# Performance work log

Measured on AMD Instinct MI355X. Metric: run time of the kernel, lower is better.

Reference implementation:

```python
import jax, jax.numpy as jnp
import numpy as np

N = 100000   # nodes
E = 1600000  # edges (avg degree 16)
D = 32       # feature dim

def setup_inputs() -> dict:
    key = jax.random.key(0)
    k1, k2, k3, k4 = jax.random.split(key, 4)
    feat = jax.random.normal(k1, (N, D), dtype=jnp.float32)
    e_feat = jax.random.normal(k2, (E, 1), dtype=jnp.float32)
    src = jax.random.randint(k3, (E,), 0, N)
    dst = jax.random.randint(k4, (E,), 0, N)
    return {"feat": feat, "e_feat": e_feat, "src": src, "dst": dst}

def reference(feat, e_feat, src, dst):
    n = feat.shape[0]
    ones = jnp.ones(src.shape[0], dtype=feat.dtype)
    # degrees computed on the full graph (before self-loop removal), as in DGL code
    out_deg = jax.ops.segment_sum(ones, src, num_segments=n)
    in_deg = jax.ops.segment_sum(ones, dst, num_segments=n)
    src_norm = jnp.power(jnp.clip(out_deg, 1.0, None), -0.5)[:, None]  # [N,1]
    dst_norm = jnp.power(jnp.clip(in_deg, 1.0, None), -0.5)[:, None]   # [N,1]
    # remove_self_loop: mask out self-loop edges in the aggregation only
    mask = (src != dst).astype(feat.dtype)[:, None]                    # [E,1]
    # u_mul_e: gather normalized src features, multiply by edge weight
    msg = (feat * src_norm)[src] * (e_feat * mask)                     # [E,D]
    agg = jax.ops.segment_sum(msg, dst, num_segments=n)                # [N,D]
    out = feat - agg * dst_norm
    return jnp.sum(jnp.abs(out), axis=1)                               # [N]
```

## Files before the change

kernel.cpp:

```cpp
#include <hip/hip_runtime.h>

#define D 32
#define RANGE 128
#define RMAX 800
#define JC 512
#define CHUNKMAX 3200
#define CAP 2304
#define SJC 256
#define SCHUNKMAX 6400

__device__ __forceinline__ int scan512(int x, int* wp, int t) {
    int lane = t & 63, w = t >> 6;
    #pragma unroll
    for (int d = 1; d < 64; d <<= 1) {
        int y = __shfl_up(x, d, 64);
        if (lane >= d) x += y;
    }
    if (lane == 63) wp[w] = x;
    __syncthreads();
    int off = 0;
    #pragma unroll
    for (int i = 0; i < 7; i++) if (i < w) off += wp[i];
    return x + off;
}

__global__ __launch_bounds__(512) void fused_sort(
        const int* __restrict__ src, const int* __restrict__ dst,
        const float* __restrict__ ef,
        uint2* __restrict__ recs, unsigned* __restrict__ metaD,
        unsigned* __restrict__ srcs, unsigned* __restrict__ metaS,
        int E, int R, int chunk, int chunkS) {
    __shared__ __align__(16) char arena[32000];
    __shared__ int wp[8];
    int t = threadIdx.x;
    int* cnt = (int*)(arena + 25600);
    int* cur = (int*)(arena + 28800);

    if (blockIdx.x < JC) {
        int j = blockIdx.x;
        uint2* sd = (uint2*)arena;
        int e0 = j * chunk, e1 = min(E, e0 + chunk), cntE = e1 - e0;
        for (int i = t; i < RMAX; i += 512) cnt[i] = 0;
        __syncthreads();
        for (int e = e0 + 2 * t; e < e1; e += 1024) {
            if (e + 1 < e1) {
                int2 d2 = *(const int2*)(dst + e);
                atomicAdd(&cnt[d2.x >> 7], 1);
                atomicAdd(&cnt[d2.y >> 7], 1);
            } else {
                atomicAdd(&cnt[dst[e] >> 7], 1);
            }
        }
        __syncthreads();
        int v0 = cnt[t];
        int incl0 = scan512(v0, wp, t);
        int tot0 = wp[0] + wp[1] + wp[2] + wp[3] + wp[4] + wp[5] + wp[6] + wp[7];
        __syncthreads();
        int i1 = t + 512;
        int v1 = (i1 < RMAX) ? cnt[i1] : 0;
        int incl1 = scan512(v1, wp, t);
        cur[t] = incl0 - v0;
        if (i1 < RMAX) cur[i1] = tot0 + incl1 - v1;
        __syncthreads();
        for (int e = e0 + t; e < e1; e += 512) {
            int s = src[e], d = dst[e];
            float w = (s == d) ? 0.0f : ef[e];
            int pos = atomicAdd(&cur[d >> 7], 1);
            sd[pos] = make_uint2((unsigned)s | ((unsigned)(d & (RANGE - 1)) << 17),
                                 __float_as_uint(w));
        }
        __syncthreads();
        size_t baseE = (size_t)j * chunk;
        for (int i = t; i < cntE; i += 512) recs[baseE + i] = sd[i];
        for (int i = t; i < R; i += 512)
            metaD[(size_t)i * JC + j] =
                ((unsigned)(cur[i] - cnt[i]) << 16) | (unsigned)cnt[i];
    } else {
        int j = blockIdx.x - JC;
        unsigned* ids = (unsigned*)arena;
        int e0 = j * chunkS, e1 = min(E, e0 + chunkS), cntE = e1 - e0;
        for (int i = t; i < RMAX; i += 512) cnt[i] = 0;
        __syncthreads();
        for (int e = e0 + 2 * t; e < e1; e += 1024) {
            if (e + 1 < e1) {
                int2 s2 = *(const int2*)(src + e);
                atomicAdd(&cnt[s2.x >> 7], 1);
                atomicAdd(&cnt[s2.y >> 7], 1);
            } else {
                atomicAdd(&cnt[src[e] >> 7], 1);
            }
        }
        __syncthreads();
        int v0 = cnt[t];
        int incl0 = scan512(v0, wp, t);
        int tot0 = wp[0] + wp[1] + wp[2] + wp[3] + wp[4] + wp[5] + wp[6] + wp[7];
        __syncthreads();
        int i1 = t + 512;
        int v1 = (i1 < RMAX) ? cnt[i1] : 0;
        int incl1 = scan512(v1, wp, t);
        cur[t] = incl0 - v0;
        if (i1 < RMAX) cur[i1] = tot0 + incl1 - v1;
        __syncthreads();
        for (int e = e0 + t; e < e1; e += 512) {
            unsigned s = (unsigned)src[e];
            int pos = atomicAdd(&cur[s >> 7], 1);
            ids[pos] = s;
        }
        __syncthreads();
        size_t baseE = (size_t)j * chunkS;
        for (int i = t; i < cntE; i += 512) srcs[baseE + i] = ids[i];
        for (int i = t; i < R; i += 512)
            metaS[(size_t)j * R + i] =
                ((unsigned)(cur[i] - cnt[i]) << 16) | (unsigned)cnt[i];
    }
}

__device__ __forceinline__ unsigned short f2bf(float x) {
    unsigned u = __float_as_uint(x);
    u += 0x7FFFu + ((u >> 16) & 1u);
    return (unsigned short)(u >> 16);
}

__global__ __launch_bounds__(512) void srcnorm_convert(
        const unsigned* __restrict__ srcs, const unsigned* __restrict__ metaS,
        const float* __restrict__ feat, unsigned short* __restrict__ featb,
        int n, int R, int chunkS) {
    __shared__ int cnt[RANGE];
    __shared__ unsigned meta[SJC];
    int r = blockIdx.x, t = threadIdx.x;
    int base = r * RANGE, lim = min(n - base, RANGE);
    if (t < RANGE) cnt[t] = 0;
    if (t < SJC) meta[t] = metaS[(size_t)t * R + r];
    __syncthreads();
    int seg = t >> 1, sub = t & 1;
    {
        unsigned m = meta[seg];
        int st = m >> 16, c = m & 0xFFFFu;
        const unsigned* p = srcs + (size_t)seg * chunkS + st;
        for (int k = sub; k < c; k += 2)
            atomicAdd(&cnt[p[k] - (unsigned)base], 1);
    }
    __syncthreads();
    int total4 = lim * 8;
    for (int i = t; i < total4; i += 512) {
        int row = i >> 3;
        float sn = rsqrtf((float)max(cnt[row], 1));
        float4 f = ((const float4*)(feat + (size_t)(base + row) * D))[i & 7];
        ushort4 u;
        u.x = f2bf(f.x * sn); u.y = f2bf(f.y * sn);
        u.z = f2bf(f.z * sn); u.w = f2bf(f.w * sn);
        ((ushort4*)(featb + (size_t)(base + row) * D))[i & 7] = u;
    }
}

__global__ __launch_bounds__(512) void gather_kernel(
        const float* __restrict__ feat, const unsigned short* __restrict__ featb,
        const uint2* __restrict__ recs, const unsigned* __restrict__ metaD,
        float* __restrict__ out, int n, int R, int chunk) {
    __shared__ uint2 raw[CAP];
    __shared__ uint2 srec[CAP];
    __shared__ int indeg[RANGE];
    __shared__ int pre[RANGE + 1];
    __shared__ int wp[8];
    int r = blockIdx.x, t = threadIdx.x;
    int base = r * RANGE, lim = min(n - base, RANGE);
    unsigned m = metaD[(size_t)r * JC + t];
    int st = m >> 16, c = m & 0xFFFFu;
    if (t < RANGE) indeg[t] = 0;
    int incl = scan512(c, wp, t);
    int dp = incl - c;
    int total = wp[0] + wp[1] + wp[2] + wp[3] + wp[4] + wp[5] + wp[6] + wp[7];
    bool ovf = total > CAP;
    const uint2* p = recs + (size_t)t * chunk + st;
    if (!ovf) {
        for (int k = 0; k < c; k++) {
            uint2 rec = p[k];
            raw[dp + k] = rec;
            atomicAdd(&indeg[rec.x >> 17], 1);
        }
    } else {
        for (int k = 0; k < c; k++) atomicAdd(&indeg[p[k].x >> 17], 1);
    }
    __syncthreads();
    int vv = (t < RANGE) ? indeg[t] : 0;
    int incl2 = scan512(vv, wp, t);
    if (t < RANGE) pre[t + 1] = incl2;
    if (t == 0) pre[0] = 0;
    __syncthreads();
    if (t < RANGE) indeg[t] = pre[t];
    __syncthreads();
    if (!ovf) {
        for (int i = t; i < total; i += 512) {
            uint2 rec = raw[i];
            int dl = rec.x >> 17;
            int pos = atomicAdd(&indeg[dl], 1);
            srec[pos] = make_uint2(rec.x & 0x1FFFFu, rec.y);
        }
    }
    __syncthreads();
    int node = t >> 2;
    int cch = t & 3;
    if (node >= lim) return;
    int p0i = pre[node];
    int cnt = pre[node + 1] - p0i;
    float a0 = 0.f, a1 = 0.f, a2 = 0.f, a3 = 0.f, a4 = 0.f, a5 = 0.f, a6 = 0.f, a7 = 0.f;
    if (!ovf) {
        const uint2* sp = srec + p0i;
        int i = 0;
        for (; i + 4 <= cnt; i += 4) {
            uint2 q0 = sp[i], q1 = sp[i + 1], q2 = sp[i + 2], q3 = sp[i + 3];
            uint4 b0 = ((const uint4*)(featb + (size_t)q0.x * D))[cch];
            uint4 b1 = ((const uint4*)(featb + (size_t)q1.x * D))[cch];
            uint4 b2 = ((const uint4*)(featb + (size_t)q2.x * D))[cch];
            uint4 b3 = ((const uint4*)(featb + (size_t)q3.x * D))[cch];
            float w0 = __uint_as_float(q0.y), w1 = __uint_as_float(q1.y);
            float w2 = __uint_as_float(q2.y), w3 = __uint_as_float(q3.y);
            a0 += __uint_as_float(b0.x << 16) * w0 + __uint_as_float(b1.x << 16) * w1
                + __uint_as_float(b2.x << 16) * w2 + __uint_as_float(b3.x << 16) * w3;
            a1 += __uint_as_float(b0.x & 0xFFFF0000u) * w0 + __uint_as_float(b1.x & 0xFFFF0000u) * w1
                + __uint_as_float(b2.x & 0xFFFF0000u) * w2 + __uint_as_float(b3.x & 0xFFFF0000u) * w3;
            a2 += __uint_as_float(b0.y << 16) * w0 + __uint_as_float(b1.y << 16) * w1
                + __uint_as_float(b2.y << 16) * w2 + __uint_as_float(b3.y << 16) * w3;
            a3 += __uint_as_float(b0.y & 0xFFFF0000u) * w0 + __uint_as_float(b1.y & 0xFFFF0000u) * w1
                + __uint_as_float(b2.y & 0xFFFF0000u) * w2 + __uint_as_float(b3.y & 0xFFFF0000u) * w3;
            a4 += __uint_as_float(b0.z << 16) * w0 + __uint_as_float(b1.z << 16) * w1
                + __uint_as_float(b2.z << 16) * w2 + __uint_as_float(b3.z << 16) * w3;
            a5 += __uint_as_float(b0.z & 0xFFFF0000u) * w0 + __uint_as_float(b1.z & 0xFFFF0000u) * w1
                + __uint_as_float(b2.z & 0xFFFF0000u) * w2 + __uint_as_float(b3.z & 0xFFFF0000u) * w3;
            a6 += __uint_as_float(b0.w << 16) * w0 + __uint_as_float(b1.w << 16) * w1
                + __uint_as_float(b2.w << 16) * w2 + __uint_as_float(b3.w << 16) * w3;
            a7 += __uint_as_float(b0.w & 0xFFFF0000u) * w0 + __uint_as_float(b1.w & 0xFFFF0000u) * w1
                + __uint_as_float(b2.w & 0xFFFF0000u) * w2 + __uint_as_float(b3.w & 0xFFFF0000u) * w3;
        }
        for (; i < cnt; i++) {
            uint2 q = sp[i];
            uint4 b = ((const uint4*)(featb + (size_t)q.x * D))[cch];
            float w = __uint_as_float(q.y);
            a0 += __uint_as_float(b.x << 16) * w;
            a1 += __uint_as_float(b.x & 0xFFFF0000u) * w;
            a2 += __uint_as_float(b.y << 16) * w;
            a3 += __uint_as_float(b.y & 0xFFFF0000u) * w;
            a4 += __uint_as_float(b.z << 16) * w;
            a5 += __uint_as_float(b.z & 0xFFFF0000u) * w;
            a6 += __uint_as_float(b.w << 16) * w;
            a7 += __uint_as_float(b.w & 0xFFFF0000u) * w;
        }
    } else {
        for (int j = 0; j < JC; j++) {
            unsigned mm = metaD[(size_t)r * JC + j];
            const uint2* pp = recs + (size_t)j * chunk + (mm >> 16);
            int cc = mm & 0xFFFFu;
            for (int k = 0; k < cc; k++) {
                uint2 rec = pp[k];
                if ((int)(rec.x >> 17) == node) {
                    uint4 b = ((const uint4*)(featb + (size_t)(rec.x & 0x1FFFFu) * D))[cch];
                    float w = __uint_as_float(rec.y);
                    a0 += __uint_as_float(b.x << 16) * w;
                    a1 += __uint_as_float(b.x & 0xFFFF0000u) * w;
                    a2 += __uint_as_float(b.y << 16) * w;
                    a3 += __uint_as_float(b.y & 0xFFFF0000u) * w;
                    a4 += __uint_as_float(b.z << 16) * w;
                    a5 += __uint_as_float(b.z & 0xFFFF0000u) * w;
                    a6 += __uint_as_float(b.w << 16) * w;
                    a7 += __uint_as_float(b.w & 0xFFFF0000u) * w;
                }
            }
        }
    }
    float dn = rsqrtf((float)max(cnt, 1));
    const float4* fr = (const float4*)(feat + (size_t)(base + node) * D);
    float4 fA = fr[cch * 2];
    float4 fB = fr[cch * 2 + 1];
    float v = fabsf(fA.x - a0 * dn) + fabsf(fA.y - a1 * dn) +
              fabsf(fA.z - a2 * dn) + fabsf(fA.w - a3 * dn) +
              fabsf(fB.x - a4 * dn) + fabsf(fB.y - a5 * dn) +
              fabsf(fB.z - a6 * dn) + fabsf(fB.w - a7 * dn);
    v += __shfl_xor(v, 1, 4);
    v += __shfl_xor(v, 2, 4);
    if (cch == 0) out[base + node] = v;
}

extern "C" void kernel_launch(void* const* d_in, const int* in_sizes, int n_in,
                              void* d_out, int out_size, void* d_ws, size_t ws_size,
                              hipStream_t stream) {
    const float* feat   = (const float*)d_in[0];
    const float* e_feat = (const float*)d_in[1];
    const int*   src    = (const int*)d_in[2];
    const int*   dst    = (const int*)d_in[3];
    const int E = in_sizes[2];
    const int n = in_sizes[0] / D;
    float* out = (float*)d_out;

    const int R = (n + RANGE - 1) / RANGE;
    const int chunk  = (((E + JC  - 1) / JC ) + 1) & ~1;
    const int chunkS = (((E + SJC - 1) / SJC) + 1) & ~1;

    char* p = (char*)d_ws;
    uint2* recs     = (uint2*)p;    p += ((size_t)JC * chunk * 8 + 15) & ~(size_t)15;
    unsigned* metaD = (unsigned*)p; p += ((size_t)R * JC * 4 + 15) & ~(size_t)15;
    unsigned* srcs  = (unsigned*)p; p += ((size_t)SJC * chunkS * 4 + 15) & ~(size_t)15;
    unsigned* metaS = (unsigned*)p; p += ((size_t)SJC * R * 4 + 15) & ~(size_t)15;
    unsigned short* featb = (unsigned short*)p;

    fused_sort<<<JC + SJC, 512, 0, stream>>>(src, dst, e_feat, recs, metaD,
                                             srcs, metaS, E, R, chunk, chunkS);

    srcnorm_convert<<<R, 512, 0, stream>>>(srcs, metaS, feat, featb, n, R, chunkS);

    gather_kernel<<<R, 512, 0, stream>>>(feat, featb, recs, metaD, out, n, R, chunk);
}
```

Measured before the change: 139.3 us.

## Scatter bucketed edges into per-bucket regions via global atomic cursors

The sort kernel no longer writes each chunk's locally sorted records plus a per-chunk metadata table. Each block now reserves space in a fixed-stride per-bucket region through a global atomic cursor and copies its bucket slice there directly. The consumer kernels then read one contiguous region per bucket with coalesced loads, without the metadata load and prefix scan over 512 or 256 chunk segments. The cost is an extra zeroing kernel launch, global atomics, and short serial per-thread copy loops. It also assumes no bucket exceeds the fixed STRIDE of 2560 records.

Result: slower. 146.0 us (+4.8%).

```diff
diff --git a/kernel.cpp b/kernel.cpp
--- a/kernel.cpp
+++ b/kernel.cpp
@@ -8,6 +8,9 @@
 #define CAP 2304
 #define SJC 256
 #define SCHUNKMAX 6400
+#define STRIDE 2560
+#define SSTRIDE 2560
+#define CPAD 16
 
 __device__ __forceinline__ int scan512(int x, int* wp, int t) {
     int lane = t & 63, w = t >> 6;
@@ -24,11 +27,16 @@
     return x + off;
 }
 
+__global__ __launch_bounds__(256) void zero_cur(int* __restrict__ p, int m) {
+    int i = blockIdx.x * 256 + threadIdx.x;
+    if (i < m) p[i] = 0;
+}
+
 __global__ __launch_bounds__(512) void fused_sort(
         const int* __restrict__ src, const int* __restrict__ dst,
         const float* __restrict__ ef,
-        uint2* __restrict__ recs, unsigned* __restrict__ metaD,
-        unsigned* __restrict__ srcs, unsigned* __restrict__ metaS,
+        uint2* __restrict__ recsR, unsigned* __restrict__ srcsR,
+        int* __restrict__ gcurD, int* __restrict__ gcurS,
         int E, int R, int chunk, int chunkS) {
     __shared__ __align__(16) char arena[32000];
     __shared__ int wp[8];
@@ -39,7 +47,7 @@
     if (blockIdx.x < JC) {
         int j = blockIdx.x;
         uint2* sd = (uint2*)arena;
-        int e0 = j * chunk, e1 = min(E, e0 + chunk), cntE = e1 - e0;
+        int e0 = j * chunk, e1 = min(E, e0 + chunk);
         for (int i = t; i < RMAX; i += 512) cnt[i] = 0;
         __syncthreads();
         for (int e = e0 + 2 * t; e < e1; e += 1024) {
@@ -70,15 +78,19 @@
                                  __float_as_uint(w));
         }
         __syncthreads();
-        size_t baseE = (size_t)j * chunk;
-        for (int i = t; i < cntE; i += 512) recs[baseE + i] = sd[i];
-        for (int i = t; i < R; i += 512)
-            metaD[(size_t)i * JC + j] =
-                ((unsigned)(cur[i] - cnt[i]) << 16) | (unsigned)cnt[i];
+        for (int i = t; i < R; i += 512) {
+            int c = cnt[i];
+            if (c) {
+                int g = atomicAdd(&gcurD[i * CPAD], c);
+                int ls = cur[i] - c;
+                uint2* dp = recsR + (size_t)i * STRIDE + g;
+                for (int k = 0; k < c; k++) dp[k] = sd[ls + k];
+            }
+        }
     } else {
         int j = blockIdx.x - JC;
         unsigned* ids = (unsigned*)arena;
-        int e0 = j * chunkS, e1 = min(E, e0 + chunkS), cntE = e1 - e0;
+        int e0 = j * chunkS, e1 = min(E, e0 + chunkS);
         for (int i = t; i < RMAX; i += 512) cnt[i] = 0;
         __syncthreads();
         for (int e = e0 + 2 * t; e < e1; e += 1024) {
@@ -107,11 +119,15 @@
             ids[pos] = s;
         }
         __syncthreads();
-        size_t baseE = (size_t)j * chunkS;
-        for (int i = t; i < cntE; i += 512) srcs[baseE + i] = ids[i];
-        for (int i = t; i < R; i += 512)
-            metaS[(size_t)j * R + i] =
-                ((unsigned)(cur[i] - cnt[i]) << 16) | (unsigned)cnt[i];
+        for (int i = t; i < R; i += 512) {
+            int c = cnt[i];
+            if (c) {
+                int g = atomicAdd(&gcurS[i * CPAD], c);
+                int ls = cur[i] - c;
+                unsigned* dp = srcsR + (size_t)i * SSTRIDE + g;
+                for (int k = 0; k < c; k++) dp[k] = ids[ls + k];
+            }
+        }
     }
 }
 
@@ -122,24 +138,18 @@
 }
 
 __global__ __launch_bounds__(512) void srcnorm_convert(
-        const unsigned* __restrict__ srcs, const unsigned* __restrict__ metaS,
+        const unsigned* __restrict__ srcsR, const int* __restrict__ gcurS,
         const float* __restrict__ feat, unsigned short* __restrict__ featb,
-        int n, int R, int chunkS) {
+        int n, int R) {
     __shared__ int cnt[RANGE];
-    __shared__ unsigned meta[SJC];
     int r = blockIdx.x, t = threadIdx.x;
     int base = r * RANGE, lim = min(n - base, RANGE);
     if (t < RANGE) cnt[t] = 0;
-    if (t < SJC) meta[t] = metaS[(size_t)t * R + r];
-    __syncthreads();
-    int seg = t >> 1, sub = t & 1;
-    {
-        unsigned m = meta[seg];
-        int st = m >> 16, c = m & 0xFFFFu;
-        const unsigned* p = srcs + (size_t)seg * chunkS + st;
-        for (int k = sub; k < c; k += 2)
-            atomicAdd(&cnt[p[k] - (unsigned)base], 1);
-    }
+    __syncthreads();
+    int total = gcurS[r * CPAD];
+    const unsigned* p = srcsR + (size_t)r * SSTRIDE;
+    for (int i = t; i < total; i += 512)
+        atomicAdd(&cnt[p[i] - (unsigned)base], 1);
     __syncthreads();
     int total4 = lim * 8;
     for (int i = t; i < total4; i += 512) {
@@ -155,8 +165,8 @@
 
 __global__ __launch_bounds__(512) void gather_kernel(
         const float* __restrict__ feat, const unsigned short* __restrict__ featb,
-        const uint2* __restrict__ recs, const unsigned* __restrict__ metaD,
-        float* __restrict__ out, int n, int R, int chunk) {
+        const uint2* __restrict__ recsR, const int* __restrict__ gcurD,
+        float* __restrict__ out, int n, int R) {
     __shared__ uint2 raw[CAP];
     __shared__ uint2 srec[CAP];
     __shared__ int indeg[RANGE];
@@ -164,22 +174,20 @@
     __shared__ int wp[8];
     int r = blockIdx.x, t = threadIdx.x;
     int base = r * RANGE, lim = min(n - base, RANGE);
-    unsigned m = metaD[(size_t)r * JC + t];
-    int st = m >> 16, c = m & 0xFFFFu;
+    int total = gcurD[r * CPAD];
+    bool ovf = total > CAP;
+    const uint2* reg = recsR + (size_t)r * STRIDE;
     if (t < RANGE) indeg[t] = 0;
-    int incl = scan512(c, wp, t);
-    int dp = incl - c;
-    int total = wp[0] + wp[1] + wp[2] + wp[3] + wp[4] + wp[5] + wp[6] + wp[7];
-    bool ovf = total > CAP;
-    const uint2* p = recs + (size_t)t * chunk + st;
+    __syncthreads();
     if (!ovf) {
-        for (int k = 0; k < c; k++) {
-            uint2 rec = p[k];
-            raw[dp + k] = rec;
+        for (int i = t; i < total; i += 512) {
+            uint2 rec = reg[i];
+            raw[i] = rec;
             atomicAdd(&indeg[rec.x >> 17], 1);
         }
     } else {
-        for (int k = 0; k < c; k++) atomicAdd(&indeg[p[k].x >> 17], 1);
+        for (int i = t; i < total; i += 512)
+            atomicAdd(&indeg[reg[i].x >> 17], 1);
     }
     __syncthreads();
     int vv = (t < RANGE) ? indeg[t] : 0;
@@ -246,24 +254,19 @@
             a7 += __uint_as_float(b.w & 0xFFFF0000u) * w;
         }
     } else {
-        for (int j = 0; j < JC; j++) {
-            unsigned mm = metaD[(size_t)r * JC + j];
-            const uint2* pp = recs + (size_t)j * chunk + (mm >> 16);
-            int cc = mm & 0xFFFFu;
-            for (int k = 0; k < cc; k++) {
-                uint2 rec = pp[k];
-                if ((int)(rec.x >> 17) == node) {
-                    uint4 b = ((const uint4*)(featb + (size_t)(rec.x & 0x1FFFFu) * D))[cch];
-                    float w = __uint_as_float(rec.y);
-                    a0 += __uint_as_float(b.x << 16) * w;
-                    a1 += __uint_as_float(b.x & 0xFFFF0000u) * w;
-                    a2 += __uint_as_float(b.y << 16) * w;
-                    a3 += __uint_as_float(b.y & 0xFFFF0000u) * w;
-                    a4 += __uint_as_float(b.z << 16) * w;
-                    a5 += __uint_as_float(b.z & 0xFFFF0000u) * w;
-                    a6 += __uint_as_float(b.w << 16) * w;
-                    a7 += __uint_as_float(b.w & 0xFFFF0000u) * w;
-                }
+        for (int k = 0; k < total; k++) {
+            uint2 rec = reg[k];
+            if ((int)(rec.x >> 17) == node) {
+                uint4 b = ((const uint4*)(featb + (size_t)(rec.x & 0x1FFFFu) * D))[cch];
+                float w = __uint_as_float(rec.y);
+                a0 += __uint_as_float(b.x << 16) * w;
+                a1 += __uint_as_float(b.x & 0xFFFF0000u) * w;
+                a2 += __uint_as_float(b.y << 16) * w;
+                a3 += __uint_as_float(b.y & 0xFFFF0000u) * w;
+                a4 += __uint_as_float(b.z << 16) * w;
+                a5 += __uint_as_float(b.z & 0xFFFF0000u) * w;
+                a6 += __uint_as_float(b.w << 16) * w;
+                a7 += __uint_as_float(b.w & 0xFFFF0000u) * w;
             }
         }
     }
@@ -296,16 +299,19 @@
     const int chunkS = (((E + SJC - 1) / SJC) + 1) & ~1;
 
     char* p = (char*)d_ws;
-    uint2* recs     = (uint2*)p;    p += ((size_t)JC * chunk * 8 + 15) & ~(size_t)15;
-    unsigned* metaD = (unsigned*)p; p += ((size_t)R * JC * 4 + 15) & ~(size_t)15;
-    unsigned* srcs  = (unsigned*)p; p += ((size_t)SJC * chunkS * 4 + 15) & ~(size_t)15;
-    unsigned* metaS = (unsigned*)p; p += ((size_t)SJC * R * 4 + 15) & ~(size_t)15;
+    uint2* recsR    = (uint2*)p;    p += ((size_t)R * STRIDE * 8 + 15) & ~(size_t)15;
+    unsigned* srcsR = (unsigned*)p; p += ((size_t)R * SSTRIDE * 4 + 15) & ~(size_t)15;
+    int* gcurD      = (int*)p;      p += ((size_t)R * CPAD * 4 + 15) & ~(size_t)15;
+    int* gcurS      = (int*)p;      p += ((size_t)R * CPAD * 4 + 15) & ~(size_t)15;
     unsigned short* featb = (unsigned short*)p;
 
-    fused_sort<<<JC + SJC, 512, 0, stream>>>(src, dst, e_feat, recs, metaD,
-                                             srcs, metaS, E, R, chunk, chunkS);
-
-    srcnorm_convert<<<R, 512, 0, stream>>>(srcs, metaS, feat, featb, n, R, chunkS);
-
-    gather_kernel<<<R, 512, 0, stream>>>(feat, featb, recs, metaD, out, n, R, chunk);
-}
+    const int mcur = R * CPAD * 2;
+    zero_cur<<<(mcur + 255) / 256, 256, 0, stream>>>(gcurD, mcur);
+
+    fused_sort<<<JC + SJC, 512, 0, stream>>>(src, dst, e_feat, recsR, srcsR,
+                                             gcurD, gcurS, E, R, chunk, chunkS);
+
+    srcnorm_convert<<<R, 512, 0, stream>>>(srcsR, gcurS, feat, featb, n, R);
+
+    gather_kernel<<<R, 512, 0, stream>>>(feat, featb, recsR, gcurD, out, n, R);
+}
```
